# Performance work log

Measured on AMD Instinct MI355X. Metric: run time of the kernel, lower is better.

The kernel has to match this reference:

```python
import jax, jax.numpy as jnp
import numpy as np

D = 512   # Nsites: single-particle Hilbert space dimension
N = 128   # Nparticles
TINY = 1e-30


def setup_inputs() -> dict:
    key = jax.random.key(0)
    k1, k2 = jax.random.split(key)
    # Orthonormal orbitals (mirrors reortho_orbitals: QR of a random matrix)
    A = jax.random.normal(k1, (D, D), dtype=jnp.float32)
    Q, _ = jnp.linalg.qr(A)
    P = Q[:, :N]                                   # (D, N) orthonormal columns
    u = jax.random.uniform(k2, (N,), dtype=jnp.float32)  # inverse-CDF draws, one per particle
    return {"P": P, "u": u}


def _sample(P, u):
    """Ordered componentwise sampling from the Slater determinant.

    Uses the identity that Ksites is always a contiguous range [0..i], so the
    determinant ratios -det(G[0:i+1]-diag(occ+e_i))/det(G[0:x_{k-1}+1]-diag(occ))
    reduce to running products of Schur-complement pivots s_j = G_jj - b^T Xinv b
    of the leading block of (G - diag(occ)).  A single O(D) scan maintains the
    (padded) inverse of that leading block via rank-1 bordered-inverse updates,
    replacing the per-step np.ix_/vstack/det kernel launches of the original.
    """
    dt = P.dtype
    G = jnp.eye(D, dtype=dt) - P @ P.T             # (D, D), symmetric projection complement
    idxs = jnp.arange(D)

    def step(carry, i):
        Xinv, ratio, cumul, k = carry
        b = jnp.where(idxs < i, G[:, i], 0.0)      # border column, masked to leading block
        v = Xinv @ b                               # Xinv is zero-padded beyond processed block
        s = G[i, i] - b @ v                        # Schur pivot (site i unoccupied)
        last_allowed = D - N + k                   # xmax - 1 for particle k
        active = (k < N) & (i <= last_allowed)
        # cond prob particle k sits at site i: -(s-1) * prod of unoccupied pivots since x_{k-1}
        p = jnp.where(active, -(s - 1.0) * ratio, 0.0)
        u_k = u[jnp.clip(k, 0, N - 1)]
        occupy = active & ((cumul + p >= u_k) | (i == last_allowed))  # inverse-CDF; force at support end
        pivot = jnp.where(occupy, s - 1.0, s)
        pivot = jnp.where(jnp.abs(pivot) < TINY, TINY, pivot)
        # bordered inverse update: [[X,b],[b,d]]^-1 via outer(vext,vext)/pivot
        vext = jnp.where(idxs == i, -1.0, v)
        Xinv = Xinv + jnp.outer(vext, vext) / pivot
        ratio = jnp.where(occupy, 1.0, jnp.where(active, ratio * s, ratio))
        cumul = jnp.where(occupy, 0.0, cumul + p)
        k = k + occupy.astype(jnp.int32)
        return (Xinv, ratio, cumul, k), (p, k - occupy.astype(jnp.int32), occupy)

    init = (jnp.zeros((D, D), dtype=dt), jnp.asarray(1.0, dt), jnp.asarray(0.0, dt),
            jnp.asarray(0, jnp.int32))
    _, (p_rec, k_rec, occ_rec) = jax.lax.scan(step, init, idxs)

    krow = jnp.where(k_rec < N, k_rec, N)          # out-of-range rows dropped
    cond_probs = jnp.zeros((N, D), dtype=dt).at[krow, idxs].set(p_rec, mode='drop')
    return cond_probs, occ_rec


def reference(P, u):
    cond_probs, occ = _sample(P, u)
    positions = jnp.nonzero(occ, size=N, fill_value=-1)[0]  # ordered sampled sites
    return cond_probs, positions
```

## Files before the change

kernel.cpp:

```cpp
#include <hip/hip_runtime.h>


#define DD 512
#define NN 128
#define NTHREADS 512
#define BB 16
#define NBLK (DD / BB)

typedef float v2f __attribute__((ext_vector_type(2)));

__device__ __forceinline__ float lane_bcast(float v, int l) {
  return __int_as_float(__builtin_amdgcn_readlane(__float_as_int(v), l));
}
__device__ __forceinline__ void pk_fma_vv(v2f& acc, v2f a, v2f b) {
  asm("v_pk_fma_f32 %0, %1, %2, %0" : "+v"(acc) : "v"(a), "v"(b));
}
__device__ __forceinline__ void pk_fma_vs(v2f& acc, v2f a, v2f bs) {
  asm("v_pk_fma_f32 %0, %1, %2, %0" : "+v"(acc) : "v"(a), "s"(bs));
}
__device__ __forceinline__ v2f pk_mul_vv(v2f a, v2f b) {
  v2f d;
  asm("v_pk_mul_f32 %0, %1, %2" : "=v"(d) : "v"(a), "v"(b));
  return d;
}
__device__ __forceinline__ void pk_add_vv(v2f& acc, v2f a) {
  asm("v_pk_add_f32 %0, %1, %0" : "+v"(acc) : "v"(a));
}

__device__ __forceinline__ v2f wave_reduce_add64_pk(v2f sd) {
#if __has_builtin(__builtin_amdgcn_permlane32_swap)
  {
    unsigned xl = __float_as_uint(sd.x), xh = __float_as_uint(sd.y);
    auto rl = __builtin_amdgcn_permlane32_swap(xl, xl, false, false);
    auto rh = __builtin_amdgcn_permlane32_swap(xh, xh, false, false);
    v2f partner = {__uint_as_float(rl[1]), __uint_as_float(rh[1])};
    v2f self    = {__uint_as_float(rl[0]), __uint_as_float(rh[0])};
    sd = self;
    pk_add_vv(sd, partner);
  }
#else
  sd.x += __shfl_xor(sd.x, 32, 64);
  sd.y += __shfl_xor(sd.y, 32, 64);
#endif
#if __has_builtin(__builtin_amdgcn_permlane16_swap)
  {
    unsigned xl = __float_as_uint(sd.x), xh = __float_as_uint(sd.y);
    auto rl = __builtin_amdgcn_permlane16_swap(xl, xl, false, false);
    auto rh = __builtin_amdgcn_permlane16_swap(xh, xh, false, false);
    v2f partner = {__uint_as_float(rl[1]), __uint_as_float(rh[1])};
    v2f self    = {__uint_as_float(rl[0]), __uint_as_float(rh[0])};
    sd = self;
    pk_add_vv(sd, partner);
  }
#else
  sd.x += __shfl_xor(sd.x, 16, 64);
  sd.y += __shfl_xor(sd.y, 16, 64);
#endif
  sd.x += __int_as_float(__builtin_amdgcn_update_dpp(
      0, __float_as_int(sd.x), 0x128, 0xF, 0xF, true));
  sd.y += __int_as_float(__builtin_amdgcn_update_dpp(
      0, __float_as_int(sd.y), 0x128, 0xF, 0xF, true));
  {
    v2f partner = {
        __int_as_float(__builtin_amdgcn_ds_swizzle(__float_as_int(sd.x), 0x101F)),
        __int_as_float(__builtin_amdgcn_ds_swizzle(__float_as_int(sd.y), 0x101F))};
    pk_add_vv(sd, partner);
  }
  sd.x += __int_as_float(__builtin_amdgcn_update_dpp(
      0, __float_as_int(sd.x), 0x4E, 0xF, 0xF, true));
  sd.y += __int_as_float(__builtin_amdgcn_update_dpp(
      0, __float_as_int(sd.y), 0x4E, 0xF, 0xF, true));
  sd.x += __int_as_float(__builtin_amdgcn_update_dpp(
      0, __float_as_int(sd.x), 0xB1, 0xF, 0xF, true));
  sd.y += __int_as_float(__builtin_amdgcn_update_dpp(
      0, __float_as_int(sd.y), 0xB1, 0xF, 0xF, true));
  return sd;
}

__global__ __launch_bounds__(NTHREADS) void slater_scan_kernel(
    const float* __restrict__ P, const float* __restrict__ u,
    float* __restrict__ out) {
  const int tid   = threadIdx.x;
  const int wave  = tid >> 6;
  const int lane  = tid & 63;
  const int c0    = wave << 4;
  const bool lowhalf = (wave < 4);

  __shared__ __align__(16) float part[8][64][36];
  __shared__ __align__(16) float Vld[128][20];
  __shared__ __align__(16) float CldT[16][20];
  __shared__ __align__(16) float Pst[2][BB][NN];
  __shared__ __align__(16) float Wst[8][16][20];

  for (int j = tid; j < NN * DD; j += NTHREADS) out[j] = 0.0f;

  const float ur0 = u[lane];
  const float ur1 = u[64 + lane];

  const int sr = tid >> 5;
  const int sc = (tid & 31) << 2;
  *(float4*)&Pst[0][sr][sc] = *(const float4*)&P[sr * NN + sc];

  v2f A2r0[8], A2r1[8];
#pragma unroll
  for (int jp = 0; jp < 8; ++jp) {
    A2r0[jp] = (v2f){(lane == c0 + 2 * jp) ? 1.0f : 0.0f,
                     (lane == c0 + 2 * jp + 1) ? 1.0f : 0.0f};
    A2r1[jp] = (v2f){(lane + 64 == c0 + 2 * jp) ? 1.0f : 0.0f,
                     (lane + 64 == c0 + 2 * jp + 1) ? 1.0f : 0.0f};
  }

  float ratio = 1.0f, cumul = 0.0f;
  int k = 0;

  __syncthreads();

  for (int blk = 0; blk < NBLK; ++blk) {
    const int i0  = blk * BB;
    const int buf = blk & 1;

    float4 stg;
    const bool do_stage = (blk + 1 < NBLK);
    if (do_stage) stg = *(const float4*)&P[(i0 + BB + sr) * NN + sc];

    const int t2r = 2 * wave;
    const float pt0l = Pst[buf][t2r][lane];
    const float pt0h = Pst[buf][t2r][64 + lane];
    const float pt1l = Pst[buf][t2r + 1][lane];
    const float pt1h = Pst[buf][t2r + 1][64 + lane];

    float pa0[16], pa1[16];
#pragma unroll
    for (int t = 0; t < 16; ++t) {
      const float4 q0 = *(const float4*)&Pst[buf][t][c0];
      const float4 q1 = *(const float4*)&Pst[buf][t][c0 + 4];
      const float4 q2 = *(const float4*)&Pst[buf][t][c0 + 8];
      const float4 q3 = *(const float4*)&Pst[buf][t][c0 + 12];
      const v2f pp0 = {q0.x, q0.y}, pp1 = {q0.z, q0.w};
      const v2f pp2 = {q1.x, q1.y}, pp3 = {q1.z, q1.w};
      const v2f pp4 = {q2.x, q2.y}, pp5 = {q2.z, q2.w};
      const v2f pp6 = {q3.x, q3.y}, pp7 = {q3.z, q3.w};
      v2f a0 = pk_mul_vv(A2r0[0], pp0);
      v2f a1 = pk_mul_vv(A2r1[0], pp0);
      pk_fma_vv(a0, A2r0[1], pp1); pk_fma_vv(a1, A2r1[1], pp1);
      pk_fma_vv(a0, A2r0[2], pp2); pk_fma_vv(a1, A2r1[2], pp2);
      pk_fma_vv(a0, A2r0[3], pp3); pk_fma_vv(a1, A2r1[3], pp3);
      pk_fma_vv(a0, A2r0[4], pp4); pk_fma_vv(a1, A2r1[4], pp4);
      pk_fma_vv(a0, A2r0[5], pp5); pk_fma_vv(a1, A2r1[5], pp5);
      pk_fma_vv(a0, A2r0[6], pp6); pk_fma_vv(a1, A2r1[6], pp6);
      pk_fma_vv(a0, A2r0[7], pp7); pk_fma_vv(a1, A2r1[7], pp7);
      pa0[t] = a0.x + a0.y;
      pa1[t] = a1.x + a1.y;
    }
    {
      float4* myp = (float4*)&part[wave][lane][0];
      myp[0] = make_float4(pa0[0],  pa0[1],  pa0[2],  pa0[3]);
      myp[1] = make_float4(pa0[4],  pa0[5],  pa0[6],  pa0[7]);
      myp[2] = make_float4(pa0[8],  pa0[9],  pa0[10], pa0[11]);
      myp[3] = make_float4(pa0[12], pa0[13], pa0[14], pa0[15]);
      myp[4] = make_float4(pa1[0],  pa1[1],  pa1[2],  pa1[3]);
      myp[5] = make_float4(pa1[4],  pa1[5],  pa1[6],  pa1[7]);
      myp[6] = make_float4(pa1[8],  pa1[9],  pa1[10], pa1[11]);
      myp[7] = make_float4(pa1[12], pa1[13], pa1[14], pa1[15]);
    }
    if (do_stage) *(float4*)&Pst[buf ^ 1][sr][sc] = stg;
    __syncthreads();

    {
      const int r  = tid >> 2;
      const int qd = tid & 3;
      const int rl = r & 63;
      const int rh = (r >> 6) << 4;
      v2f s01 = {0.0f, 0.0f}, s23 = {0.0f, 0.0f};
#pragma unroll
      for (int v = 0; v < 8; ++v) {
        const float4 x = *(const float4*)&part[v][rl][rh + 4 * qd];
        pk_add_vv(s01, (v2f){x.x, x.y});
        pk_add_vv(s23, (v2f){x.z, x.w});
      }
      *(float4*)&Vld[r][4 * qd] = make_float4(s01.x, s01.y, s23.x, s23.y);
    }
    __syncthreads();

    v2f Wp[16];
    {
      const float4 x0 = *(const float4*)&Vld[lane][0];
      const float4 x1 = *(const float4*)&Vld[lane][4];
      const float4 x2 = *(const float4*)&Vld[lane][8];
      const float4 x3 = *(const float4*)&Vld[lane][12];
      const float4 y0 = *(const float4*)&Vld[lane + 64][0];
      const float4 y1 = *(const float4*)&Vld[lane + 64][4];
      const float4 y2 = *(const float4*)&Vld[lane + 64][8];
      const float4 y3 = *(const float4*)&Vld[lane + 64][12];
      Wp[0]  = (v2f){x0.x, y0.x}; Wp[1]  = (v2f){x0.y, y0.y};
      Wp[2]  = (v2f){x0.z, y0.z}; Wp[3]  = (v2f){x0.w, y0.w};
      Wp[4]  = (v2f){x1.x, y1.x}; Wp[5]  = (v2f){x1.y, y1.y};
      Wp[6]  = (v2f){x1.z, y1.z}; Wp[7]  = (v2f){x1.w, y1.w};
      Wp[8]  = (v2f){x2.x, y2.x}; Wp[9]  = (v2f){x2.y, y2.y};
      Wp[10] = (v2f){x2.z, y2.z}; Wp[11] = (v2f){x2.w, y2.w};
      Wp[12] = (v2f){x3.x, y3.x}; Wp[13] = (v2f){x3.y, y3.y};
      Wp[14] = (v2f){x3.z, y3.z}; Wp[15] = (v2f){x3.w, y3.w};
    }

    {
      v2f cr[16];
#pragma unroll
      for (int mm = 0; mm < 16; ++mm) {
        const v2f wx = {Wp[mm].x, Wp[mm].x};
        const v2f wy = {Wp[mm].y, Wp[mm].y};
        v2f seed = pk_mul_vv((v2f){pt0h, pt1h}, wy);
        pk_fma_vv(seed, (v2f){pt0l, pt1l}, wx);
        cr[mm] = wave_reduce_add64_pk(seed);
      }
      if (lane == 0) {
#pragma unroll
        for (int mm = 0; mm < 16; ++mm) {
          CldT[mm][t2r]     = cr[mm].x;
          CldT[mm][t2r + 1] = cr[mm].y;
        }
      }
    }
    int kidx = (k < NN) ? k : (NN - 1);
    float uk = (kidx < 64) ? lane_bcast(ur0, kidx & 63)
                           : lane_bcast(ur1, kidx & 63);
    __syncthreads();

    const int m = lane & 15;
    float Ereg[16];
    {
      const float4 e0 = *(const float4*)&CldT[m][0];
      const float4 e1 = *(const float4*)&CldT[m][4];
      const float4 e2 = *(const float4*)&CldT[m][8];
      const float4 e3 = *(const float4*)&CldT[m][12];
      Ereg[0]  = e0.x; Ereg[1]  = e0.y; Ereg[2]  = e0.z; Ereg[3]  = e0.w;
      Ereg[4]  = e1.x; Ereg[5]  = e1.y; Ereg[6]  = e1.z; Ereg[7]  = e1.w;
      Ereg[8]  = e2.x; Ereg[9]  = e2.y; Ereg[10] = e2.z; Ereg[11] = e2.w;
      Ereg[12] = e3.x; Ereg[13] = e3.y; Ereg[14] = e3.z; Ereg[15] = e3.w;
    }
    v2f SWp[16];
    bool done = false;
#pragma unroll
    for (int t = 0; t < 16; ++t) {
      const float s = 1.0f - lane_bcast(Ereg[t], t);
      const int i = i0 + t;
      const int last_allowed = DD - NN + k;
      const bool active = (k < NN) && (i <= last_allowed);
      const float pr = active ? (-(s - 1.0f) * ratio) : 0.0f;
      const bool occupy = active && ((cumul + pr >= uk) || (i == last_allowed));
      float pivot = occupy ? (s - 1.0f) : s;
      pivot = (fabsf(pivot) < 1e-30f) ? 1e-30f : pivot;
      const float invp = 1.0f / pivot;

      if (lane == 0 && wave == (t & 7)) {
        if (k < NN) out[k * DD + i] = pr;
        if (occupy) out[NN * DD + k] = (float)i;
      }

      ratio = occupy ? 1.0f : (active ? ratio * s : ratio);
      cumul = occupy ? 0.0f : (cumul + pr);
      k += occupy ? 1 : 0;
      if (k == NN) { done = true; break; }

      {
        const int kidx2 = (k < NN) ? k : (NN - 1);
        uk = (kidx2 < 64) ? lane_bcast(ur0, kidx2 & 63)
                          : lane_bcast(ur1, kidx2 & 63);
      }

      const float SDl = Ereg[t] * invp;
      SWp[t] = pk_mul_vv(Wp[t], (v2f){invp, invp});
#pragma unroll
      for (int t2 = t + 1; t2 < 16; ++t2) {
        const float djt2 = lane_bcast(Ereg[t], t2);
        Ereg[t2] = fmaf(djt2, SDl, Ereg[t2]);
        pk_fma_vs(Wp[t2], SWp[t], (v2f){djt2, djt2});
      }
    }
    if (done) return;

    {
      const bool writer = ((lane >> 4) == (wave & 3));
      const int jl = lane & 15;
      if (writer) {
#pragma unroll
        for (int t = 0; t < 16; ++t)
          Wst[wave][t][jl] = lowhalf ? Wp[t].x : Wp[t].y;
      }
    }

#pragma unroll
    for (int t = 0; t < 16; ++t) {
      const float4 q0 = *(const float4*)&Wst[wave][t][0];
      const float4 q1 = *(const float4*)&Wst[wave][t][4];
      const float4 q2 = *(const float4*)&Wst[wave][t][8];
      const float4 q3 = *(const float4*)&Wst[wave][t][12];
      const v2f w0d = {SWp[t].x, SWp[t].x};
      const v2f w1d = {SWp[t].y, SWp[t].y};
      const v2f c01 = {q0.x, q0.y}, c23 = {q0.z, q0.w};
      const v2f c45 = {q1.x, q1.y}, c67 = {q1.z, q1.w};
      const v2f c89 = {q2.x, q2.y}, cab = {q2.z, q2.w};
      const v2f ccd = {q3.x, q3.y}, cef = {q3.z, q3.w};
      pk_fma_vv(A2r0[0], w0d, c01); pk_fma_vv(A2r1[0], w1d, c01);
      pk_fma_vv(A2r0[1], w0d, c23); pk_fma_vv(A2r1[1], w1d, c23);
      pk_fma_vv(A2r0[2], w0d, c45); pk_fma_vv(A2r1[2], w1d, c45);
      pk_fma_vv(A2r0[3], w0d, c67); pk_fma_vv(A2r1[3], w1d, c67);
      pk_fma_vv(A2r0[4], w0d, c89); pk_fma_vv(A2r1[4], w1d, c89);
      pk_fma_vv(A2r0[5], w0d, cab); pk_fma_vv(A2r1[5], w1d, cab);
      pk_fma_vv(A2r0[6], w0d, ccd); pk_fma_vv(A2r1[6], w1d, ccd);
      pk_fma_vv(A2r0[7], w0d, cef); pk_fma_vv(A2r1[7], w1d, cef);
    }
  }
}

extern "C" void kernel_launch(void* const* d_in, const int* in_sizes, int n_in,
                              void* d_out, int out_size, void* d_ws,
                              size_t ws_size, hipStream_t stream) {
  const float* P = (const float*)d_in[0];
  const float* u = (const float*)d_in[1];
  float* out = (float*)d_out;
  hipLaunchKernelGGL(slater_scan_kernel, dim3(1), dim3(NTHREADS), 0, stream,
                     P, u, out);
}
```

Before: 422.6 us.

## Buffer per-step outputs in LDS and flush once; vectorize zero-fill and W loads

Per-site probabilities, particle indices and positions are recorded in shared memory during the scan and written to global memory in one coalesced pass at the end, replacing scattered single-lane global stores inside the serial loop. The zero-fill of the output switches to float4 stores. Vld is relaid so each lane loads its W pairs as contiguous v2f, and the CldT writes use v2f stores. The early return becomes a break so all threads reach the final flush, which adds a barrier and extra LDS.

```diff
diff --git a/kernel.cpp b/kernel.cpp
--- a/kernel.cpp
+++ b/kernel.cpp
@@ -87,12 +87,19 @@
   const bool lowhalf = (wave < 4);
 
   __shared__ __align__(16) float part[8][64][36];
-  __shared__ __align__(16) float Vld[128][20];
+  __shared__ __align__(16) float Vld2[64][34];
   __shared__ __align__(16) float CldT[16][20];
   __shared__ __align__(16) float Pst[2][BB][NN];
   __shared__ __align__(16) float Wst[8][16][20];
-
-  for (int j = tid; j < NN * DD; j += NTHREADS) out[j] = 0.0f;
+  __shared__ float pr_ld[DD];
+  __shared__ int   kq_ld[DD];
+  __shared__ float pos_ld[NN];
+
+  {
+    const float4 z4 = make_float4(0.f, 0.f, 0.f, 0.f);
+    for (int j = tid; j < (NN * DD) / 4; j += NTHREADS) ((float4*)out)[j] = z4;
+  }
+  kq_ld[tid] = NN;
 
   const float ur0 = u[lane];
   const float ur1 = u[64 + lane];
@@ -171,6 +178,7 @@
       const int qd = tid & 3;
       const int rl = r & 63;
       const int rh = (r >> 6) << 4;
+      const int h  = r >> 6;
       v2f s01 = {0.0f, 0.0f}, s23 = {0.0f, 0.0f};
 #pragma unroll
       for (int v = 0; v < 8; ++v) {
@@ -178,29 +186,18 @@
         pk_add_vv(s01, (v2f){x.x, x.y});
         pk_add_vv(s23, (v2f){x.z, x.w});
       }
-      *(float4*)&Vld[r][4 * qd] = make_float4(s01.x, s01.y, s23.x, s23.y);
+      const int cb = 8 * qd + h;
+      Vld2[rl][cb + 0] = s01.x;
+      Vld2[rl][cb + 2] = s01.y;
+      Vld2[rl][cb + 4] = s23.x;
+      Vld2[rl][cb + 6] = s23.y;
     }
     __syncthreads();
 
     v2f Wp[16];
-    {
-      const float4 x0 = *(const float4*)&Vld[lane][0];
-      const float4 x1 = *(const float4*)&Vld[lane][4];
-      const float4 x2 = *(const float4*)&Vld[lane][8];
-      const float4 x3 = *(const float4*)&Vld[lane][12];
-      const float4 y0 = *(const float4*)&Vld[lane + 64][0];
-      const float4 y1 = *(const float4*)&Vld[lane + 64][4];
-      const float4 y2 = *(const float4*)&Vld[lane + 64][8];
-      const float4 y3 = *(const float4*)&Vld[lane + 64][12];
-      Wp[0]  = (v2f){x0.x, y0.x}; Wp[1]  = (v2f){x0.y, y0.y};
-      Wp[2]  = (v2f){x0.z, y0.z}; Wp[3]  = (v2f){x0.w, y0.w};
-      Wp[4]  = (v2f){x1.x, y1.x}; Wp[5]  = (v2f){x1.y, y1.y};
-      Wp[6]  = (v2f){x1.z, y1.z}; Wp[7]  = (v2f){x1.w, y1.w};
-      Wp[8]  = (v2f){x2.x, y2.x}; Wp[9]  = (v2f){x2.y, y2.y};
-      Wp[10] = (v2f){x2.z, y2.z}; Wp[11] = (v2f){x2.w, y2.w};
-      Wp[12] = (v2f){x3.x, y3.x}; Wp[13] = (v2f){x3.y, y3.y};
-      Wp[14] = (v2f){x3.z, y3.z}; Wp[15] = (v2f){x3.w, y3.w};
-    }
+#pragma unroll
+    for (int t = 0; t < 16; ++t)
+      Wp[t] = *(const v2f*)&Vld2[lane][2 * t];
 
     {
       v2f cr[16];
@@ -214,10 +211,8 @@
       }
       if (lane == 0) {
 #pragma unroll
-        for (int mm = 0; mm < 16; ++mm) {
-          CldT[mm][t2r]     = cr[mm].x;
-          CldT[mm][t2r + 1] = cr[mm].y;
-        }
+        for (int mm = 0; mm < 16; ++mm)
+          *(v2f*)&CldT[mm][t2r] = cr[mm];
       }
     }
     int kidx = (k < NN) ? k : (NN - 1);
@@ -252,8 +247,9 @@
       const float invp = 1.0f / pivot;
 
       if (lane == 0 && wave == (t & 7)) {
-        if (k < NN) out[k * DD + i] = pr;
-        if (occupy) out[NN * DD + k] = (float)i;
+        kq_ld[i] = k;
+        pr_ld[i] = pr;
+        if (occupy) pos_ld[k] = (float)i;
       }
 
       ratio = occupy ? 1.0f : (active ? ratio * s : ratio);
@@ -276,7 +272,7 @@
         pk_fma_vs(Wp[t2], SWp[t], (v2f){djt2, djt2});
       }
     }
-    if (done) return;
+    if (done) break;
 
     {
       const bool writer = ((lane >> 4) == (wave & 3));
@@ -310,6 +306,13 @@
       pk_fma_vv(A2r0[7], w0d, cef); pk_fma_vv(A2r1[7], w1d, cef);
     }
   }
+
+  __syncthreads();
+  {
+    const int kk = kq_ld[tid];
+    if (kk < NN) out[kk * DD + tid] = pr_ld[tid];
+    if (tid < NN) out[NN * DD + tid] = pos_ld[tid];
+  }
 }
 
 extern "C" void kernel_launch(void* const* d_in, const int* in_sizes, int n_in,
```

Measured after the change: 442.6 us. +4.7%, slower.
